# Kernel tuning notes

Measured on AMD Instinct MI355X. Metric: run time of the kernel, lower is better.

The kernel has to match this reference:

```python
import jax, jax.numpy as jnp
import numpy as np

B, T, D, H, C, S = 1024, 64, 512, 512, 96, 21  # batch, enc_len, input_size, hidden, num_classes, decode steps


def setup_inputs() -> dict:
    key = jax.random.key(0)
    ks = jax.random.split(key, 12)
    sc = lambda n: 1.0 / np.sqrt(n)
    return {
        "batch_H": jax.random.normal(ks[0], (B, T, D), jnp.float32),
        "text": jax.random.randint(ks[1], (B, S), 0, C),
        "Wi": jax.random.normal(ks[2], (H, D), jnp.float32) * sc(D),
        "Wh": jax.random.normal(ks[3], (H, H), jnp.float32) * sc(H),
        "bh": jax.random.normal(ks[4], (H,), jnp.float32) * sc(H),
        "Ws": jax.random.normal(ks[5], (1, H), jnp.float32) * sc(H),
        "Wih": jax.random.normal(ks[6], (4 * H, D + C), jnp.float32) * sc(H),
        "Whh": jax.random.normal(ks[7], (4 * H, H), jnp.float32) * sc(H),
        "bih": jax.random.normal(ks[8], (4 * H,), jnp.float32) * sc(H),
        "bhh": jax.random.normal(ks[9], (4 * H,), jnp.float32) * sc(H),
        "Wg": jax.random.normal(ks[10], (C, H), jnp.float32) * sc(H),
        "bg": jax.random.normal(ks[11], (C,), jnp.float32) * sc(H),
    }


def reference(batch_H, text, Wi, Wh, bh, Ws, Wih, Whh, bih, bhh, Wg, bg):
    # Teacher-forced (is_train=True) path; dropout is identity (eval mode / p=0).
    # Precompute i2h(batch_H) once -- the per-step result is identical.
    Hp = jnp.einsum('btd,hd->bth', batch_H, Wi)  # [B,T,H]
    onehots = jax.nn.one_hot(text, C, dtype=batch_H.dtype)  # [B,S,C]

    def step(carry, oh):
        h, c = carry
        ph = h @ Wh.T + bh                              # h2h(prev_hidden[0])  [B,H]
        e = jnp.tanh(Hp + ph[:, None, :]) @ Ws[0]       # score -> [B,T]
        alpha = jax.nn.softmax(e, axis=1)               # softmax over enc steps
        ctx = jnp.einsum('bt,btd->bd', alpha, batch_H)  # bmm context  [B,D]
        x = jnp.concatenate([ctx, oh], axis=1)          # [B, D+C]
        gates = x @ Wih.T + bih + h @ Whh.T + bhh       # LSTMCell gates [B,4H]
        i_g, f_g, g_g, o_g = jnp.split(gates, 4, axis=1)  # torch gate order i,f,g,o
        c2 = jax.nn.sigmoid(f_g) * c + jax.nn.sigmoid(i_g) * jnp.tanh(g_g)
        h2 = jax.nn.sigmoid(o_g) * jnp.tanh(c2)
        return (h2, c2), h2

    init = (jnp.zeros((B, H), batch_H.dtype), jnp.zeros((B, H), batch_H.dtype))
    _, hs = jax.lax.scan(step, init, jnp.swapaxes(onehots, 0, 1))  # hs: [S,B,H]
    output_hiddens = jnp.swapaxes(hs, 0, 1)                        # [B,S,H]
    probs = output_hiddens @ Wg.T + bg                             # generator [B,S,C]
    return probs
```

## Files before the change

kernel.cpp:

```cpp
#include <hip/hip_runtime.h>
#include <hip/hip_bf16.h>
#include <math.h>

using bf16 = __hip_bfloat16;

#define NB 1024
#define NT 64
#define ND 512
#define NH 512
#define NC 96
#define NS 21
#define NDC 608
#define NG 2048

#define OFF_HPB   0u
#define OFF_BHB   16777216u
#define OFF_C     33554432u
#define OFF_HB16  34078720u
#define OFF_CTXB  34865152u
#define OFF_WCB   35127296u
#define OFF_WIH2  35291136u
#define OFF_HB2   36339712u
#define OFF_WIB   37224448u
#define OFF_BH_   38569984u
#define OFF_WS_   38570496u
#define OFF_BG_   38571008u
#define OFF_OH    38571104u
#define OFF_PHP   38767712u
#define WS_NEED_FLOATS 44010592u
#define WS_NEED_BYTES ((size_t)WS_NEED_FLOATS * 4u)

typedef __attribute__((ext_vector_type(8))) short bf16x8;
typedef __attribute__((ext_vector_type(4))) float f32x4;

__device__ __forceinline__ unsigned short f2bu(float f) {
    unsigned u = __float_as_uint(f);
    unsigned r = (u + 0x7fffu + ((u >> 16) & 1u)) >> 16;
    return (unsigned short)r;
}
__device__ __forceinline__ float b2f(short s) {
    return __uint_as_float(((unsigned)(unsigned short)s) << 16);
}
__device__ __forceinline__ float fast_sigmoid(float x) {
    return __builtin_amdgcn_rcpf(1.f + __expf(-x));
}
__device__ __forceinline__ float fast_tanh(float x) {
    return 1.f - 2.f * __builtin_amdgcn_rcpf(1.f + __expf(2.f * x));
}

#define BH_BLOCKS 32768u
#define W_ELEMS   2884704u
#define W_BLOCKS  ((W_ELEMS + 255u) / 256u)

__global__ __launch_bounds__(256) void conv_all(
    const float* __restrict__ bHsrc,
    const float* __restrict__ Wi, const float* __restrict__ Wh, const float* __restrict__ bh,
    const float* __restrict__ Ws, const float* __restrict__ Wih, const float* __restrict__ Whh,
    const float* __restrict__ bih, const float* __restrict__ bhh, const float* __restrict__ Wg,
    const float* __restrict__ bg, float* __restrict__ ws) {
    if (blockIdx.x < BH_BLOCKS) {
        unsigned short* dst = (unsigned short*)(ws + OFF_BHB);
        size_t i = ((size_t)blockIdx.x * 256 + threadIdx.x) * 4;
        float4 v = *(const float4*)(bHsrc + i);
        uint2 pk;
        pk.x = (unsigned)f2bu(v.x) | ((unsigned)f2bu(v.y) << 16);
        pk.y = (unsigned)f2bu(v.z) | ((unsigned)f2bu(v.w) << 16);
        *(uint2*)&dst[i] = pk;
        return;
    }
    unsigned i = (blockIdx.x - BH_BLOCKS) * 256u + threadIdx.x;
    if (i >= W_ELEMS) return;
    unsigned short* WiB  = (unsigned short*)(ws + OFF_WIB);
    unsigned short* WcB  = (unsigned short*)(ws + OFF_WCB);
    unsigned short* Wih2 = (unsigned short*)(ws + OFF_WIH2);
    if (i < 262144u) {
        WiB[i] = f2bu(Wi[i]);
    } else if (i < 524288u) {
        unsigned j = i - 262144u;
        WcB[j] = f2bu(Wh[j]);
    } else if (i < 573440u) {
        unsigned j = i - 524288u;
        WcB[262144u + j] = f2bu(Wg[j]);
    } else if (i < 589824u) {
        unsigned j = i - 573440u;
        WcB[311296u + j] = 0;
    } else if (i < 1638400u) {
        unsigned j = i - 589824u;
        unsigned row = j >> 9, col = j & 511u;
        Wih2[row * 1024u + col] = f2bu(Wih[(size_t)row * NDC + col]);
    } else if (i < 2686976u) {
        unsigned j = i - 1638400u;
        unsigned row = j >> 9, col = j & 511u;
        Wih2[row * 1024u + 512u + col] = f2bu(Whh[j]);
    } else if (i < 2687488u) {
        unsigned j = i - 2686976u;
        ws[OFF_BH_ + j] = bh[j];
    } else if (i < 2688000u) {
        unsigned j = i - 2687488u;
        ws[OFF_WS_ + j] = Ws[j];
    } else if (i < 2688096u) {
        unsigned j = i - 2688000u;
        ws[OFF_BG_ + j] = bg[j];
    } else {
        unsigned j = i - 2688096u;
        unsigned c = j >> 11, n = j & 2047u;
        ws[OFF_OH + j] = Wih[(size_t)n * NDC + ND + c] + bih[n] + bhh[n];
    }
}

__global__ __launch_bounds__(256) void hp_gemm(const bf16* __restrict__ A,
                                               const bf16* __restrict__ B,
                                               bf16* __restrict__ outB) {
    __shared__ short As[128 * 40];
    __shared__ short Bs[128 * 40];
    const int tid = threadIdx.x;
    const int wave = tid >> 6, lane = tid & 63;
    const int wrow = wave >> 1, wcol = wave & 1;
    const int quad = lane >> 4, l16 = lane & 15;
    const int m0 = blockIdx.x * 128, n0 = blockIdx.y * 128;
    f32x4 acc[4][4];
    #pragma unroll
    for (int mi = 0; mi < 4; ++mi)
        #pragma unroll
        for (int ni = 0; ni < 4; ++ni) acc[mi][ni] = (f32x4){0.f, 0.f, 0.f, 0.f};
    for (int k0 = 0; k0 < 512; k0 += 32) {
        #pragma unroll
        for (int l = 0; l < 2; ++l) {
            int c = tid + l * 256;
            int row = c >> 2, c8 = c & 3;
            *(uint4*)&As[row * 40 + c8 * 8] =
                *(const uint4*)&A[(size_t)(m0 + row) * 512 + k0 + c8 * 8];
            *(uint4*)&Bs[row * 40 + c8 * 8] =
                *(const uint4*)&B[(size_t)(n0 + row) * 512 + k0 + c8 * 8];
        }
        __syncthreads();
        bf16x8 af[4], bfr[4];
        #pragma unroll
        for (int mi = 0; mi < 4; ++mi)
            af[mi] = *(const bf16x8*)&As[(wrow * 64 + mi * 16 + l16) * 40 + quad * 8];
        #pragma unroll
        for (int ni = 0; ni < 4; ++ni)
            bfr[ni] = *(const bf16x8*)&Bs[(wcol * 64 + ni * 16 + l16) * 40 + quad * 8];
        #pragma unroll
        for (int mi = 0; mi < 4; ++mi)
            #pragma unroll
            for (int ni = 0; ni < 4; ++ni)
                acc[mi][ni] = __builtin_amdgcn_mfma_f32_16x16x32_bf16(af[mi], bfr[ni],
                                                                      acc[mi][ni], 0, 0, 0);
        __syncthreads();
    }
    #pragma unroll
    for (int mi = 0; mi < 4; ++mi)
        #pragma unroll
        for (int ni = 0; ni < 4; ++ni)
            #pragma unroll
            for (int r = 0; r < 4; ++r) {
                int m = m0 + wrow * 64 + mi * 16 + quad * 4 + r;
                int n = n0 + wcol * 64 + ni * 16 + l16;
                outB[(size_t)m * 512 + n] = __float2bfloat16(acc[mi][ni][r]);
            }
}

__global__ __launch_bounds__(256) void attn_phase(
    const bf16* __restrict__ Hp, const bf16* __restrict__ bH,
    const float* __restrict__ bh, const float* __restrict__ bg,
    const float* __restrict__ Wsv, const float* __restrict__ php,
    unsigned short* __restrict__ ctxB, float* __restrict__ out, int s) {
    const int b = blockIdx.x;
    const int tid = threadIdx.x;
    const int wave = tid >> 6, lane = tid & 63;
    __shared__ float smem[6304];
    float* tr = smem;
    float* red = smem + 4160;
    float* salpha = smem + 6240;
    float ph8[8];
    #pragma unroll
    for (int j = 0; j < 8; ++j) ph8[j] = bh[lane * 8 + j];
    if (s > 0) {
        #pragma unroll
        for (int p = 0; p < 8; ++p) {
            const float* src = php + ((size_t)b * 8 + p) * 640 + lane * 8;
            float4 x = *(const float4*)src, y = *(const float4*)(src + 4);
            ph8[0] += x.x; ph8[1] += x.y; ph8[2] += x.z; ph8[3] += x.w;
            ph8[4] += y.x; ph8[5] += y.y; ph8[6] += y.z; ph8[7] += y.w;
        }
        if (tid < NC) {
            float v = bg[tid];
            #pragma unroll
            for (int p = 0; p < 8; ++p)
                v += php[((size_t)b * 8 + p) * 640 + 512 + tid];
            out[(size_t)b * (NS * NC) + (s - 1) * NC + tid] = v;
        }
    }
    float ws8[8];
    {
        float4 wsa = *(const float4*)(Wsv + lane * 8);
        float4 wsb = *(const float4*)(Wsv + lane * 8 + 4);
        ws8[0] = wsa.x; ws8[1] = wsa.y; ws8[2] = wsa.z; ws8[3] = wsa.w;
        ws8[4] = wsb.x; ws8[5] = wsb.y; ws8[6] = wsb.z; ws8[7] = wsb.w;
    }
    const bf16* hpb = Hp + ((size_t)b * NT + wave * 16) * NH + lane * 8;
    #pragma unroll
    for (int i = 0; i < 16; ++i) {
        bf16x8 hv = *(const bf16x8*)(hpb + (size_t)i * NH);
        float sc = 0.f;
        #pragma unroll
        for (int j = 0; j < 8; ++j) sc += fast_tanh(b2f(hv[j]) + ph8[j]) * ws8[j];
        tr[(wave * 16 + i) * 65 + lane] = sc;
    }
    __syncthreads();
    {
        int t = tid & 63, ch = tid >> 6;
        const float* row = &tr[t * 65 + ch * 16];
        float pp = 0.f;
        #pragma unroll
        for (int j = 0; j < 16; ++j) pp += row[j];
        red[ch * 520 + t] = pp;
    }
    __syncthreads();
    if (tid < NT) {
        float e = red[tid] + red[520 + tid] + red[1040 + tid] + red[1560 + tid];
        float m = e;
        #pragma unroll
        for (int off = 32; off > 0; off >>= 1) m = fmaxf(m, __shfl_xor(m, off, 64));
        float exv = __expf(e - m);
        float ssum = exv;
        #pragma unroll
        for (int off = 32; off > 0; off >>= 1) ssum += __shfl_xor(ssum, off, 64);
        salpha[tid] = exv / ssum;
    }
    __syncthreads();
    {
        const bf16* bhp = bH + ((size_t)b * NT + wave * 16) * ND + lane * 8;
        float a8[8];
        #pragma unroll
        for (int u = 0; u < 8; ++u) a8[u] = 0.f;
        #pragma unroll
        for (int i = 0; i < 16; ++i) {
            float al = salpha[wave * 16 + i];
            bf16x8 v = *(const bf16x8*)(bhp + (size_t)i * ND);
            #pragma unroll
            for (int u = 0; u < 8; ++u) a8[u] = fmaf(al, b2f(v[u]), a8[u]);
        }
        #pragma unroll
        for (int u = 0; u < 8; ++u) red[wave * 520 + lane * 8 + u] = a8[u];
    }
    __syncthreads();
    for (int d = tid; d < ND; d += 256) {
        float sum = red[d] + red[520 + d] + red[1040 + d] + red[1560 + d];
        ctxB[(size_t)b * ND + d] = f2bu(sum);
    }
}

__global__ __launch_bounds__(256) void gates_phase(
    const bf16* __restrict__ ctxB, const bf16* __restrict__ hIn,
    const bf16* __restrict__ Wih2, const bf16* __restrict__ WcB,
    const float* __restrict__ ohb, const int* __restrict__ text, int s,
    float* __restrict__ c, unsigned short* __restrict__ hOut,
    float* __restrict__ php) {
    __shared__ float smem[12672];
    short* lds = (short*)smem;
    float* ex = smem;
    short* hlds = (short*)((char*)smem + 46080);
    const int tid = threadIdx.x;
    const int wave = tid >> 6, lane = tid & 63;
    const int quad = lane >> 4, l16 = lane & 15;
    const int g = wave;
    const int m0 = (blockIdx.x >> 3) * 32;
    const int p = blockIdx.x & 7;
    const int kp0 = p * 64;
    const int arow = tid >> 2, ac8 = tid & 3;
    const short* Wih2s = (const short*)Wih2;
    f32x4 acc[2][4];
    #pragma unroll
    for (int mi = 0; mi < 2; ++mi)
        #pragma unroll
        for (int ni = 0; ni < 4; ++ni) acc[mi][ni] = (f32x4){0.f, 0.f, 0.f, 0.f};

    uint4 rb[4]; uint4 ra;
#define STAGE_LOAD(K0)                                                         \
    {                                                                          \
        _Pragma("unroll")                                                      \
        for (int l = 0; l < 4; ++l) {                                          \
            int j = tid + l * 256;                                             \
            int row = j >> 2, c8 = j & 3;                                      \
            int brow = (row >> 6) * 512 + kp0 + (row & 63);                    \
            rb[l] = *(const uint4*)&Wih2s[(size_t)brow * 1024 + (K0) + c8 * 8];\
        }                                                                      \
        if (tid < 128) {                                                       \
            const short* srcA = ((K0) < 512)                                   \
                ? (const short*)ctxB + (size_t)(m0 + arow) * 512 + (K0) + ac8 * 8          \
                : (const short*)hIn + (size_t)(m0 + arow) * 512 + ((K0) - 512) + ac8 * 8;  \
            ra = *(const uint4*)srcA;                                          \
        }                                                                      \
    }
#define STAGE_WRITE(BUF)                                                       \
    {                                                                          \
        _Pragma("unroll")                                                      \
        for (int l = 0; l < 4; ++l) {                                          \
            int j = tid + l * 256;                                             \
            int row = j >> 2, c8 = j & 3;                                      \
            *(uint4*)&lds[(BUF) * 11520 + 1280 + row * 40 + c8 * 8] = rb[l];   \
        }                                                                      \
        if (tid < 128) *(uint4*)&lds[(BUF) * 11520 + arow * 40 + ac8 * 8] = ra;\
    }

    STAGE_LOAD(0);
    STAGE_WRITE(0);
    __syncthreads();
    for (int it = 0; it < 32; ++it) {
        const int buf = it & 1;
        if (it + 1 < 32) STAGE_LOAD((it + 1) * 32);
        bf16x8 af[2], bfr[4];
        #pragma unroll
        for (int mi = 0; mi < 2; ++mi)
            af[mi] = *(const bf16x8*)&lds[buf * 11520 + (mi * 16 + l16) * 40 + quad * 8];
        #pragma unroll
        for (int ni = 0; ni < 4; ++ni)
            bfr[ni] = *(const bf16x8*)&lds[buf * 11520 + 1280 +
                                           (g * 64 + ni * 16 + l16) * 40 + quad * 8];
        #pragma unroll
        for (int mi = 0; mi < 2; ++mi)
            #pragma unroll
            for (int ni = 0; ni < 4; ++ni)
                acc[mi][ni] = __builtin_amdgcn_mfma_f32_16x16x32_bf16(
                    af[mi], bfr[ni], acc[mi][ni], 0, 0, 0);
        if (it + 1 < 32) STAGE_WRITE(buf ^ 1);
        __syncthreads();
    }
#undef STAGE_LOAD
#undef STAGE_WRITE
    #pragma unroll
    for (int mi = 0; mi < 2; ++mi)
        #pragma unroll
        for (int ni = 0; ni < 4; ++ni)
            #pragma unroll
            for (int r = 0; r < 4; ++r) {
                int ml = mi * 16 + quad * 4 + r;
                int nl = ni * 16 + l16;
                ex[g * 2080 + ml * 65 + nl] = acc[mi][ni][r];
            }
    __syncthreads();
    #pragma unroll 1
    for (int t = 0; t < 8; ++t) {
        int idx = tid + t * 256;
        int ml = idx >> 6, kl = idx & 63;
        int m = m0 + ml, kp = kp0 + kl;
        int tb = text[m * NS + s];
        const float* oh = ohb + (size_t)tb * NG;
        float ig = fast_sigmoid(ex[0 * 2080 + ml * 65 + kl] + oh[kp]);
        float fg = fast_sigmoid(ex[1 * 2080 + ml * 65 + kl] + oh[NH + kp]);
        float gg = fast_tanh(ex[2 * 2080 + ml * 65 + kl] + oh[2 * NH + kp]);
        float og = fast_sigmoid(ex[3 * 2080 + ml * 65 + kl] + oh[3 * NH + kp]);
        float cn = fg * c[(size_t)m * NH + kp] + ig * gg;
        float hn = og * fast_tanh(cn);
        c[(size_t)m * NH + kp] = cn;
        unsigned short hb = f2bu(hn);
        hOut[(size_t)m * NH + kp] = hb;
        hlds[ml * 72 + kl] = (short)hb;
    }
    __syncthreads();
    #pragma unroll 1
    for (int nf = 0; nf < 10; ++nf) {
        int n0 = wave * 160 + nf * 16;
        f32x4 a0 = (f32x4){0.f, 0.f, 0.f, 0.f}, a1 = a0;
        #pragma unroll
        for (int ks = 0; ks < 2; ++ks) {
            bf16x8 bfrg = *(const bf16x8*)((const short*)WcB +
                (size_t)(n0 + l16) * 512 + kp0 + ks * 32 + quad * 8);
            bf16x8 af0 = *(const bf16x8*)&hlds[l16 * 72 + ks * 32 + quad * 8];
            bf16x8 af1 = *(const bf16x8*)&hlds[(16 + l16) * 72 + ks * 32 + quad * 8];
            a0 = __builtin_amdgcn_mfma_f32_16x16x32_bf16(af0, bfrg, a0, 0, 0, 0);
            a1 = __builtin_amdgcn_mfma_f32_16x16x32_bf16(af1, bfrg, a1, 0, 0, 0);
        }
        #pragma unroll
        for (int r = 0; r < 4; ++r) {
            php[((size_t)(m0 + quad * 4 + r) * 8 + p) * 640 + n0 + l16] = a0[r];
            php[((size_t)(m0 + 16 + quad * 4 + r) * 8 + p) * 640 + n0 + l16] = a1[r];
        }
    }
}

__global__ __launch_bounds__(128) void probs_final(const float* __restrict__ php,
                                                   const float* __restrict__ bg,
                                                   float* __restrict__ out) {
    const int b = blockIdx.x;
    const int tid = threadIdx.x;
    if (tid < NC) {
        float v = bg[tid];
        #pragma unroll
        for (int p = 0; p < 8; ++p) v += php[((size_t)b * 8 + p) * 640 + 512 + tid];
        out[(size_t)b * (NS * NC) + 20 * NC + tid] = v;
    }
}

extern "C" void kernel_launch(void* const* d_in, const int* in_sizes, int n_in,
                              void* d_out, int out_size, void* d_ws, size_t ws_size,
                              hipStream_t stream) {
    if (ws_size < WS_NEED_BYTES) {
        hipMemsetAsync(d_out, 0x7F, (size_t)out_size * 4, stream);
        return;
    }
    float* ws = (float*)d_ws;
    bf16* HpB  = (bf16*)(ws + OFF_HPB);
    bf16* bHB  = (bf16*)(ws + OFF_BHB);
    float* cb  = ws + OFF_C;
    bf16* h0   = (bf16*)(ws + OFF_HB16);
    bf16* h1   = (bf16*)(ws + OFF_HB2);
    bf16* ctxB = (bf16*)(ws + OFF_CTXB);
    bf16* WcB  = (bf16*)(ws + OFF_WCB);
    bf16* Wih2 = (bf16*)(ws + OFF_WIH2);
    bf16* WiB  = (bf16*)(ws + OFF_WIB);
    const int* text = (const int*)d_in[1];
    float* out = (float*)d_out;

    conv_all<<<BH_BLOCKS + W_BLOCKS, 256, 0, stream>>>(
        (const float*)d_in[0],
        (const float*)d_in[2], (const float*)d_in[3], (const float*)d_in[4],
        (const float*)d_in[5], (const float*)d_in[6], (const float*)d_in[7],
        (const float*)d_in[8], (const float*)d_in[9], (const float*)d_in[10],
        (const float*)d_in[11], ws);
    hipMemsetAsync(cb, 0, (size_t)786432 * 4, stream);

    hp_gemm<<<dim3(NB * NT / 128, ND / 128), 256, 0, stream>>>(bHB, WiB, HpB);

    for (int s = 0; s < NS; ++s) {
        bf16* hcur = (s & 1) ? h1 : h0;
        bf16* hnext = (s & 1) ? h0 : h1;
        attn_phase<<<NB, 256, 0, stream>>>(HpB, bHB, ws + OFF_BH_, ws + OFF_BG_,
                                           ws + OFF_WS_, ws + OFF_PHP,
                                           (unsigned short*)ctxB, out, s);
        gates_phase<<<dim3(256), 256, 0, stream>>>(
            ctxB, hcur, Wih2, WcB, ws + OFF_OH, text, s, cb,
            (unsigned short*)hnext, ws + OFF_PHP);
    }
    probs_final<<<NB, 128, 0, stream>>>(ws + OFF_PHP, ws + OFF_BG_, out);
}
```

Before: 1.378 ms.

## Widen attention kernel to 512 threads and prescale tanh inputs by two

Result: no change. 1.371 ms (-0.5%).

```diff
diff --git a/kernel.cpp b/kernel.cpp
--- a/kernel.cpp
+++ b/kernel.cpp
@@ -47,6 +47,9 @@
 __device__ __forceinline__ float fast_tanh(float x) {
     return 1.f - 2.f * __builtin_amdgcn_rcpf(1.f + __expf(2.f * x));
 }
+__device__ __forceinline__ float tanh_pre2(float x2) {
+    return 1.f - 2.f * __builtin_amdgcn_rcpf(1.f + __expf(x2));
+}
 
 #define BH_BLOCKS 32768u
 #define W_ELEMS   2884704u
@@ -74,10 +77,10 @@
     unsigned short* WcB  = (unsigned short*)(ws + OFF_WCB);
     unsigned short* Wih2 = (unsigned short*)(ws + OFF_WIH2);
     if (i < 262144u) {
-        WiB[i] = f2bu(Wi[i]);
+        WiB[i] = f2bu(2.f * Wi[i]);
     } else if (i < 524288u) {
         unsigned j = i - 262144u;
-        WcB[j] = f2bu(Wh[j]);
+        WcB[j] = f2bu(2.f * Wh[j]);
     } else if (i < 573440u) {
         unsigned j = i - 524288u;
         WcB[262144u + j] = f2bu(Wg[j]);
@@ -94,7 +97,7 @@
         Wih2[row * 1024u + 512u + col] = f2bu(Whh[j]);
     } else if (i < 2687488u) {
         unsigned j = i - 2686976u;
-        ws[OFF_BH_ + j] = bh[j];
+        ws[OFF_BH_ + j] = 2.f * bh[j];
     } else if (i < 2688000u) {
         unsigned j = i - 2687488u;
         ws[OFF_WS_ + j] = Ws[j];
@@ -161,65 +164,67 @@
             }
 }
 
-__global__ __launch_bounds__(256) void attn_phase(
+__global__ __launch_bounds__(512, 8) void attn_phase(
     const bf16* __restrict__ Hp, const bf16* __restrict__ bH,
-    const float* __restrict__ bh, const float* __restrict__ bg,
+    const float* __restrict__ bh2, const float* __restrict__ bg,
     const float* __restrict__ Wsv, const float* __restrict__ php,
     unsigned short* __restrict__ ctxB, float* __restrict__ out, int s) {
     const int b = blockIdx.x;
     const int tid = threadIdx.x;
     const int wave = tid >> 6, lane = tid & 63;
-    __shared__ float smem[6304];
-    float* tr = smem;
-    float* red = smem + 4160;
-    float* salpha = smem + 6240;
-    float ph8[8];
-    #pragma unroll
-    for (int j = 0; j < 8; ++j) ph8[j] = bh[lane * 8 + j];
-    if (s > 0) {
-        #pragma unroll
-        for (int p = 0; p < 8; ++p) {
-            const float* src = php + ((size_t)b * 8 + p) * 640 + lane * 8;
-            float4 x = *(const float4*)src, y = *(const float4*)(src + 4);
-            ph8[0] += x.x; ph8[1] += x.y; ph8[2] += x.z; ph8[3] += x.w;
-            ph8[4] += y.x; ph8[5] += y.y; ph8[6] += y.z; ph8[7] += y.w;
-        }
-        if (tid < NC) {
-            float v = bg[tid];
+    __shared__ float tr[64 * 65];
+    __shared__ float red[8 * 520];
+    __shared__ float phs[512];
+    __shared__ float salpha[64];
+    {
+        float v = bh2[tid];
+        if (s > 0) {
             #pragma unroll
             for (int p = 0; p < 8; ++p)
-                v += php[((size_t)b * 8 + p) * 640 + 512 + tid];
-            out[(size_t)b * (NS * NC) + (s - 1) * NC + tid] = v;
-        }
-    }
-    float ws8[8];
+                v += php[((size_t)b * 8 + p) * 640 + tid];
+        }
+        phs[tid] = v;
+        if (s > 0 && tid < NC) {
+            float pv = bg[tid];
+            #pragma unroll
+            for (int p = 0; p < 8; ++p)
+                pv += php[((size_t)b * 8 + p) * 640 + 512 + tid];
+            out[(size_t)b * (NS * NC) + (s - 1) * NC + tid] = pv;
+        }
+    }
+    __syncthreads();
+    float ph8[8], ws8[8];
+    #pragma unroll
+    for (int j = 0; j < 8; ++j) ph8[j] = phs[lane * 8 + j];
     {
         float4 wsa = *(const float4*)(Wsv + lane * 8);
         float4 wsb = *(const float4*)(Wsv + lane * 8 + 4);
         ws8[0] = wsa.x; ws8[1] = wsa.y; ws8[2] = wsa.z; ws8[3] = wsa.w;
         ws8[4] = wsb.x; ws8[5] = wsb.y; ws8[6] = wsb.z; ws8[7] = wsb.w;
     }
-    const bf16* hpb = Hp + ((size_t)b * NT + wave * 16) * NH + lane * 8;
-    #pragma unroll
-    for (int i = 0; i < 16; ++i) {
+    const bf16* hpb = Hp + ((size_t)b * NT + wave * 8) * NH + lane * 8;
+    #pragma unroll
+    for (int i = 0; i < 8; ++i) {
         bf16x8 hv = *(const bf16x8*)(hpb + (size_t)i * NH);
         float sc = 0.f;
         #pragma unroll
-        for (int j = 0; j < 8; ++j) sc += fast_tanh(b2f(hv[j]) + ph8[j]) * ws8[j];
-        tr[(wave * 16 + i) * 65 + lane] = sc;
+        for (int j = 0; j < 8; ++j) sc += tanh_pre2(b2f(hv[j]) + ph8[j]) * ws8[j];
+        tr[(wave * 8 + i) * 65 + lane] = sc;
     }
     __syncthreads();
     {
         int t = tid & 63, ch = tid >> 6;
-        const float* row = &tr[t * 65 + ch * 16];
+        const float* row = &tr[t * 65 + ch * 8];
         float pp = 0.f;
         #pragma unroll
-        for (int j = 0; j < 16; ++j) pp += row[j];
+        for (int j = 0; j < 8; ++j) pp += row[j];
         red[ch * 520 + t] = pp;
     }
     __syncthreads();
     if (tid < NT) {
-        float e = red[tid] + red[520 + tid] + red[1040 + tid] + red[1560 + tid];
+        float e = 0.f;
+        #pragma unroll
+        for (int ch = 0; ch < 8; ++ch) e += red[ch * 520 + tid];
         float m = e;
         #pragma unroll
         for (int off = 32; off > 0; off >>= 1) m = fmaxf(m, __shfl_xor(m, off, 64));
@@ -231,13 +236,13 @@
     }
     __syncthreads();
     {
-        const bf16* bhp = bH + ((size_t)b * NT + wave * 16) * ND + lane * 8;
+        const bf16* bhp = bH + ((size_t)b * NT + wave * 8) * ND + lane * 8;
         float a8[8];
         #pragma unroll
         for (int u = 0; u < 8; ++u) a8[u] = 0.f;
         #pragma unroll
-        for (int i = 0; i < 16; ++i) {
-            float al = salpha[wave * 16 + i];
+        for (int i = 0; i < 8; ++i) {
+            float al = salpha[wave * 8 + i];
             bf16x8 v = *(const bf16x8*)(bhp + (size_t)i * ND);
             #pragma unroll
             for (int u = 0; u < 8; ++u) a8[u] = fmaf(al, b2f(v[u]), a8[u]);
@@ -246,9 +251,11 @@
         for (int u = 0; u < 8; ++u) red[wave * 520 + lane * 8 + u] = a8[u];
     }
     __syncthreads();
-    for (int d = tid; d < ND; d += 256) {
-        float sum = red[d] + red[520 + d] + red[1040 + d] + red[1560 + d];
-        ctxB[(size_t)b * ND + d] = f2bu(sum);
+    {
+        float sum = 0.f;
+        #pragma unroll
+        for (int w = 0; w < 8; ++w) sum += red[w * 520 + tid];
+        ctxB[(size_t)b * ND + tid] = f2bu(sum);
     }
 }
 
@@ -427,7 +434,7 @@
     for (int s = 0; s < NS; ++s) {
         bf16* hcur = (s & 1) ? h1 : h0;
         bf16* hnext = (s & 1) ? h0 : h1;
-        attn_phase<<<NB, 256, 0, stream>>>(HpB, bHB, ws + OFF_BH_, ws + OFF_BG_,
+        attn_phase<<<NB, 512, 0, stream>>>(HpB, bHB, ws + OFF_BH_, ws + OFF_BG_,
                                            ws + OFF_WS_, ws + OFF_PHP,
                                            (unsigned short*)ctxB, out, s);
         gates_phase<<<dim3(256), 256, 0, stream>>>(
```
